# Kernel optimization log

Hardware: AMD Instinct MI355X
Metric: run time of the kernel (lower is better)

Reference implementation:

```python
import jax, jax.numpy as jnp
import numpy as np

N = 4096      # number of nodes/tokens (no batch dim in source)
D = 1024      # hidden_dim
H = 16        # n_heads
HD = D // H   # head_dim = 64
LN_EPS = 1e-5


def setup_inputs() -> dict:
    key = jax.random.key(0)
    ks = jax.random.split(key, 18)
    s = 0.02
    h = jax.random.normal(ks[0], (N, D), jnp.float32)
    rel_pos = jax.random.normal(ks[1], (N, N, 3), jnp.float32)
    # Linear weights stored (in, out) so y = x @ W + b (equiv to torch x @ W.T)
    Wq = jax.random.normal(ks[2], (D, D), jnp.float32) * s
    bq = jnp.zeros((D,), jnp.float32)
    Wk = jax.random.normal(ks[3], (D, D), jnp.float32) * s
    bk = jnp.zeros((D,), jnp.float32)
    Wv = jax.random.normal(ks[4], (D, D), jnp.float32) * s
    bv = jnp.zeros((D,), jnp.float32)
    Wo = jax.random.normal(ks[5], (D, D), jnp.float32) * s
    bo = jnp.zeros((D,), jnp.float32)
    # coord_mlp: Linear(D, D//2) -> SiLU -> Linear(D//2, 1)
    W1 = jax.random.normal(ks[6], (D, D // 2), jnp.float32) * s
    b1 = jnp.zeros((D // 2,), jnp.float32)
    W2 = jax.random.normal(ks[7], (D // 2, 1), jnp.float32) * s
    b2 = jnp.zeros((1,), jnp.float32)
    ln_w = jnp.ones((D,), jnp.float32)
    ln_b = jnp.zeros((D,), jnp.float32)
    return {"h": h, "rel_pos": rel_pos, "Wq": Wq, "bq": bq, "Wk": Wk, "bk": bk,
            "Wv": Wv, "bv": bv, "Wo": Wo, "bo": bo, "W1": W1, "b1": b1,
            "W2": W2, "b2": b2, "ln_w": ln_w, "ln_b": ln_b}


def reference(h, rel_pos, Wq, bq, Wk, bk, Wv, bv, Wo, bo, W1, b1, W2, b2, ln_w, ln_b):
    q = (h @ Wq + bq).reshape(-1, H, HD)
    k = (h @ Wk + bk).reshape(-1, H, HD)
    v = (h @ Wv + bv).reshape(-1, H, HD)
    scores = jnp.einsum('nhd,mhd->nmh', q, k) / np.sqrt(HD)  # [N, N, H]
    # Faithful to source: softmax over dim=-1 == the HEADS axis (quirk of the module)
    attn = jax.nn.softmax(scores, axis=-1)
    out = jnp.einsum('nmh,mhd->nhd', attn, v).reshape(-1, H * HD)
    out = out @ Wo + bo
    x = h + out
    mu = jnp.mean(x, axis=-1, keepdims=True)
    var = jnp.mean(jnp.square(x - mu), axis=-1, keepdims=True)
    hn = (x - mu) / jnp.sqrt(var + LN_EPS) * ln_w + ln_b
    coord_weights = jax.nn.silu(hn @ W1 + b1) @ W2 + b2   # [N, 1]
    pos_update = coord_weights * jnp.mean(rel_pos, axis=1)  # [N, 3]
    return (hn, pos_update)
```

## Files before the change

### kernel.cpp

```cpp
#include <hip/hip_runtime.h>

typedef __bf16 bf16x8 __attribute__((ext_vector_type(8)));
typedef float  f4     __attribute__((ext_vector_type(4)));
typedef unsigned short u16;
typedef unsigned short u16x4 __attribute__((ext_vector_type(4)));
typedef unsigned short u16x8 __attribute__((ext_vector_type(8)));

#define DEV __device__ __forceinline__

DEV u16 f2bf(float x) {
  unsigned u = __float_as_uint(x);
  unsigned r = u + 0x7FFFu + ((u >> 16) & 1u);
  return (u16)(r >> 16);
}
DEV float bf2f(u16 h) { return __uint_as_float(((unsigned)h) << 16); }

typedef const __attribute__((address_space(1))) void gv_t;
typedef __attribute__((address_space(3))) void lv_t;
DEV void g2l16(const void* g, void* l) {
  __builtin_amdgcn_global_load_lds((gv_t*)g, (lv_t*)l, 16, 0, 0);
}

__global__ void split_kernel(const float* __restrict__ src,
                             u16* __restrict__ hi, u16* __restrict__ lo) {
  size_t i = (size_t)blockIdx.x * 256 + threadIdx.x;
  float4 v = ((const float4*)src)[i];
  u16x4 h, l;
  u16 a;
  a = f2bf(v.x); h[0] = a; l[0] = f2bf(v.x - bf2f(a));
  a = f2bf(v.y); h[1] = a; l[1] = f2bf(v.y - bf2f(a));
  a = f2bf(v.z); h[2] = a; l[2] = f2bf(v.z - bf2f(a));
  a = f2bf(v.w); h[3] = a; l[3] = f2bf(v.w - bf2f(a));
  ((u16x4*)hi)[i] = h; ((u16x4*)lo)[i] = l;
}

__global__ void wsplit_t_kernel(const float* __restrict__ W,
                                u16* __restrict__ th, u16* __restrict__ tl, int J) {
  int j0 = blockIdx.x * 64, k0 = blockIdx.y * 64;
  __shared__ float tile[64][68];
  int t = threadIdx.x;
  int r16 = t >> 4, q = t & 15;
#pragma unroll
  for (int p = 0; p < 4; ++p) {
    int kk = r16 + p * 16;
    float4 v = *(const float4*)(W + (size_t)(k0 + kk) * J + j0 + q * 4);
    tile[kk][q * 4 + 0] = v.x; tile[kk][q * 4 + 1] = v.y;
    tile[kk][q * 4 + 2] = v.z; tile[kk][q * 4 + 3] = v.w;
  }
  __syncthreads();
  int rr = t >> 2, cq = t & 3;
  u16x8 h0, h1, l0, l1;
#pragma unroll
  for (int i = 0; i < 8; ++i) {
    float v = tile[cq * 16 + i][rr];
    u16 hh = f2bf(v); h0[i] = hh; l0[i] = f2bf(v - bf2f(hh));
    float v2 = tile[cq * 16 + 8 + i][rr];
    u16 hb = f2bf(v2); h1[i] = hb; l1[i] = f2bf(v2 - bf2f(hb));
  }
  size_t ob = (size_t)(j0 + rr) * 1024 + k0 + cq * 16;
  *(u16x8*)(th + ob) = h0; *(u16x8*)(th + ob + 8) = h1;
  *(u16x8*)(tl + ob) = l0; *(u16x8*)(tl + ob + 8) = l1;
}

template <int EPI>
__global__ __launch_bounds__(256, 2) void gemm_split_kernel(
    const u16* __restrict__ Ahi, const u16* __restrict__ Alo,
    const u16* __restrict__ Bthi, const u16* __restrict__ Btlo,
    float* __restrict__ Cf, u16* __restrict__ Cbf,
    const float* __restrict__ bias0, const float* __restrict__ bias1,
    const float* __restrict__ bias2, const float* __restrict__ Hres) {
  __shared__ alignas(16) u16 a_lds[2][4096];
  __shared__ alignas(16) u16 b_lds[2][4096];
  int t = threadIdx.x, l = t & 63, w = t >> 6;
  int wr = w >> 1, wc = w & 1, lr = l & 15, g = l >> 4;
  int m0 = blockIdx.y * 128, n0 = blockIdx.x * 128;

  f4 acc[4][4];
#pragma unroll
  for (int i = 0; i < 4; ++i)
#pragma unroll
    for (int j = 0; j < 4; ++j) acc[i][j] = (f4){0.f, 0.f, 0.f, 0.f};

  auto stage = [&](int s, int buf) {
    int p = s >> 5, k0 = (s & 31) * 32;
    const u16* As = (p < 2) ? Ahi : Alo;
    const u16* Bs = (p == 1) ? Btlo : Bthi;
#pragma unroll
    for (int i = 0; i < 2; ++i) {
      int idx = t + i * 256, r = idx >> 2, c = idx & 3;
      g2l16(As + (size_t)(m0 + r) * 1024 + k0 + 8 * (c ^ (r & 3)), &a_lds[buf][idx * 8]);
    }
#pragma unroll
    for (int i = 0; i < 2; ++i) {
      int idx = t + i * 256, r = idx >> 2, c = idx & 3;
      g2l16(Bs + (size_t)(n0 + r) * 1024 + k0 + 8 * (c ^ (r & 3)), &b_lds[buf][idx * 8]);
    }
  };

  stage(0, 0);
  for (int s = 0; s < 96; ++s) {
    __syncthreads();
    if (s + 1 < 96) stage(s + 1, (s + 1) & 1);
    const u16* ab = a_lds[s & 1];
    const u16* bb = b_lds[s & 1];
    bf16x8 af[4], bf[4];
#pragma unroll
    for (int mt = 0; mt < 4; ++mt) {
      int row = wr * 64 + mt * 16 + lr;
      af[mt] = *(const bf16x8*)(ab + row * 32 + 8 * (g ^ (row & 3)));
    }
#pragma unroll
    for (int nt = 0; nt < 4; ++nt) {
      int row = wc * 64 + nt * 16 + lr;
      bf[nt] = *(const bf16x8*)(bb + row * 32 + 8 * (g ^ (row & 3)));
    }
#pragma unroll
    for (int mt = 0; mt < 4; ++mt)
#pragma unroll
      for (int nt = 0; nt < 4; ++nt)
        acc[mt][nt] = __builtin_amdgcn_mfma_f32_16x16x32_bf16(af[mt], bf[nt], acc[mt][nt], 0, 0, 0);
  }

#pragma unroll
  for (int mt = 0; mt < 4; ++mt)
#pragma unroll
    for (int nt = 0; nt < 4; ++nt) {
      int col = n0 + wc * 64 + nt * 16 + lr;
#pragma unroll
      for (int r = 0; r < 4; ++r) {
        int row = m0 + wr * 64 + mt * 16 + 4 * g + r;
        float v = acc[mt][nt][r];
        if (EPI == 0) {
          float b = (col < 1024) ? bias0[col] : (col < 2048 ? bias1[col - 1024] : bias2[col - 2048]);
          v += b;
          if (col < 1024) v *= 0.125f;
          Cbf[(size_t)row * 3072 + col] = f2bf(v);
        } else if (EPI == 1) {
          v += bias0[col] + Hres[(size_t)row * 1024 + col];
          Cf[(size_t)row * 1024 + col] = v;
        } else {
          v += bias0[col];
          Cf[(size_t)row * 512 + col] = v;
        }
      }
    }
}

__global__ void kv_retile_kernel(const u16* __restrict__ qkvs,
                                 u16* __restrict__ kt, u16* __restrict__ vt2) {
  int mblk = blockIdx.x, t = threadIdx.x;
  __shared__ alignas(16) u16 lds[16][1032];
#pragma unroll
  for (int p = 0; p < 8; ++p) {
    int idx = t + p * 256, r = idx >> 7, c8 = idx & 127;
    *(u16x8*)(&lds[r][c8 * 8]) =
        *(const u16x8*)(qkvs + (size_t)(mblk * 16 + r) * 3072 + 1024 + c8 * 8);
  }
  __syncthreads();
#pragma unroll
  for (int p = 0; p < 8; ++p) {
    int ch = t + p * 256, cc = ch >> 4, m = ch & 15;
    u16x8 v = *(const u16x8*)(&lds[m][cc * 8]);
    *(u16x8*)(kt + (size_t)mblk * 16384 + cc * 128 + m * 8) = v;
  }
  __syncthreads();
#pragma unroll
  for (int p = 0; p < 8; ++p) {
    int idx = t + p * 256, r = idx >> 7, c8 = idx & 127;
    *(u16x8*)(&lds[r][c8 * 8]) =
        *(const u16x8*)(qkvs + (size_t)(mblk * 16 + r) * 3072 + 2048 + c8 * 8);
  }
  __syncthreads();
#pragma unroll
  for (int p = 0; p < 8; ++p) {
    int ch = t + p * 256, row = ch >> 1, half = ch & 1;
    u16x8 v;
#pragma unroll
    for (int i = 0; i < 8; ++i) v[i] = lds[half * 8 + i][row];
    *(u16x8*)(vt2 + (size_t)mblk * 16384 + row * 16 + half * 8) = v;
  }
}

__global__ __launch_bounds__(512, 2) void attn_kernel(
    const u16* __restrict__ qkvs, const u16* __restrict__ kt,
    const u16* __restrict__ vt2, float* __restrict__ out_part) {
  int t = threadIdx.x, l = t & 63, w = t >> 6;
  int nsub = w >> 2, grp = w & 3, lr = l & 15, g = l >> 4;
  int b = blockIdx.x, n0 = (b >> 1) * 32, mhalf = b & 1;
  int nrow = n0 + nsub * 16 + lr;

  __shared__ float zbuf[2][4][16][16];

  bf16x8 qf[4][2];
#pragma unroll
  for (int hh = 0; hh < 4; ++hh)
#pragma unroll
    for (int ks = 0; ks < 2; ++ks)
      qf[hh][ks] = *(const bf16x8*)(qkvs + (size_t)nrow * 3072 + (grp * 4 + hh) * 64 + ks * 32 + 8 * g);

  f4 oacc[4][4];
#pragma unroll
  for (int i = 0; i < 4; ++i)
#pragma unroll
    for (int j = 0; j < 4; ++j) oacc[i][j] = (f4){0.f, 0.f, 0.f, 0.f};

  float* opb = out_part + (size_t)mhalf * 1024 * 4096;

  for (int step = 0; step < 128; ++step) {
    int mblk = mhalf * 128 + step;
    const u16* ktb = kt + (size_t)mblk * 16384;
    const u16* vtb = vt2 + (size_t)mblk * 16384;

    u16x4 va[4][4];
#pragma unroll
    for (int hh = 0; hh < 4; ++hh)
#pragma unroll
      for (int dc = 0; dc < 4; ++dc) {
        int vrow = (grp * 4 + hh) * 64 + dc * 16 + lr;
        va[hh][dc] = *(const u16x4*)(vtb + vrow * 16 + 4 * g);
      }

    f4 sacc[4];
#pragma unroll
    for (int hh = 0; hh < 4; ++hh) sacc[hh] = (f4){0.f, 0.f, 0.f, 0.f};
#pragma unroll
    for (int ks = 0; ks < 2; ++ks) {
      bf16x8 kf[4];
#pragma unroll
      for (int hh = 0; hh < 4; ++hh) {
        int cc = (grp * 4 + hh) * 8 + ks * 4 + g;
        kf[hh] = *(const bf16x8*)(ktb + (cc * 16 + lr) * 8);
      }
#pragma unroll
      for (int hh = 0; hh < 4; ++hh)
        sacc[hh] = __builtin_amdgcn_mfma_f32_16x16x32_bf16(kf[hh], qf[hh][ks], sacc[hh], 0, 0, 0);
    }

    float ep[4][4], zp[4] = {0.f, 0.f, 0.f, 0.f};
#pragma unroll
    for (int hh = 0; hh < 4; ++hh)
#pragma unroll
      for (int r = 0; r < 4; ++r) {
        float e = __expf(sacc[hh][r]);
        ep[hh][r] = e; zp[r] += e;
      }
#pragma unroll
    for (int r = 0; r < 4; ++r) zbuf[nsub][grp][4 * g + r][lr] = zp[r];

    asm volatile("s_waitcnt lgkmcnt(0)" ::: "memory");
    __builtin_amdgcn_sched_barrier(0);
    __builtin_amdgcn_s_barrier();

    float invz[4];
#pragma unroll
    for (int r = 0; r < 4; ++r) {
      float z = zbuf[nsub][0][4 * g + r][lr] + zbuf[nsub][1][4 * g + r][lr] +
                zbuf[nsub][2][4 * g + r][lr] + zbuf[nsub][3][4 * g + r][lr];
      invz[r] = 1.0f / z;
    }

#pragma unroll
    for (int hh = 0; hh < 4; ++hh) {
      u16x8 pbu = (u16x8){0, 0, 0, 0, 0, 0, 0, 0};
      pbu[0] = f2bf(ep[hh][0] * invz[0]);
      pbu[1] = f2bf(ep[hh][1] * invz[1]);
      pbu[2] = f2bf(ep[hh][2] * invz[2]);
      pbu[3] = f2bf(ep[hh][3] * invz[3]);
      bf16x8 pb = __builtin_bit_cast(bf16x8, pbu);
#pragma unroll
      for (int dc = 0; dc < 4; ++dc) {
        u16x8 au = (u16x8){0, 0, 0, 0, 0, 0, 0, 0};
        au[0] = va[hh][dc][0]; au[1] = va[hh][dc][1];
        au[2] = va[hh][dc][2]; au[3] = va[hh][dc][3];
        bf16x8 af = __builtin_bit_cast(bf16x8, au);
        oacc[hh][dc] = __builtin_amdgcn_mfma_f32_16x16x32_bf16(af, pb, oacc[hh][dc], 0, 0, 0);
      }
    }
    asm volatile("s_waitcnt lgkmcnt(0)" ::: "memory");
    __builtin_amdgcn_sched_barrier(0);
    __builtin_amdgcn_s_barrier();
  }

#pragma unroll
  for (int hh = 0; hh < 4; ++hh)
#pragma unroll
    for (int dc = 0; dc < 4; ++dc)
#pragma unroll
      for (int r = 0; r < 4; ++r) {
        int c = (grp * 4 + hh) * 64 + dc * 16 + 4 * g + r;
        opb[(size_t)c * 4096 + nrow] = oacc[hh][dc][r];
      }
}

__global__ void combine_kernel(const float* __restrict__ part,
                               u16* __restrict__ aoh, u16* __restrict__ aol) {
  int n0 = blockIdx.x * 64, c0 = blockIdx.y * 64;
  __shared__ float tl[64][68];
  int t = threadIdx.x;
  int r16 = t >> 4, q = t & 15;
#pragma unroll
  for (int p = 0; p < 4; ++p) {
    int cc = r16 + p * 16;
    size_t off = (size_t)(c0 + cc) * 4096 + n0 + q * 4;
    float4 v0 = *(const float4*)(part + off);
    float4 v1 = *(const float4*)(part + 4194304u + off);
    tl[cc][q * 4 + 0] = v0.x + v1.x;
    tl[cc][q * 4 + 1] = v0.y + v1.y;
    tl[cc][q * 4 + 2] = v0.z + v1.z;
    tl[cc][q * 4 + 3] = v0.w + v1.w;
  }
  __syncthreads();
  int rr = t >> 2, cq = t & 3;
  u16x8 h0, h1, l0, l1;
#pragma unroll
  for (int i = 0; i < 8; ++i) {
    float v = tl[cq * 16 + i][rr];
    u16 hh = f2bf(v); h0[i] = hh; l0[i] = f2bf(v - bf2f(hh));
    float v2 = tl[cq * 16 + 8 + i][rr];
    u16 hb = f2bf(v2); h1[i] = hb; l1[i] = f2bf(v2 - bf2f(hb));
  }
  size_t ob = (size_t)(n0 + rr) * 1024 + c0 + cq * 16;
  *(u16x8*)(aoh + ob) = h0; *(u16x8*)(aoh + ob + 8) = h1;
  *(u16x8*)(aol + ob) = l0; *(u16x8*)(aol + ob + 8) = l1;
}

__global__ __launch_bounds__(256) void ln_kernel(
    const float* __restrict__ x, const float* __restrict__ lnw,
    const float* __restrict__ lnb, float* __restrict__ hn_out,
    u16* __restrict__ hnh, u16* __restrict__ hnl) {
  int row = blockIdx.x, t = threadIdx.x;
  const float* xr = x + (size_t)row * 1024;
  float4 v = *(const float4*)(xr + t * 4);
  float s = v.x + v.y + v.z + v.w;
  float sq = v.x * v.x + v.y * v.y + v.z * v.z + v.w * v.w;
#pragma unroll
  for (int o = 32; o > 0; o >>= 1) { s += __shfl_down(s, o); sq += __shfl_down(sq, o); }
  __shared__ float red[8];
  __shared__ float mv[2];
  if ((t & 63) == 0) { red[t >> 6] = s; red[4 + (t >> 6)] = sq; }
  __syncthreads();
  if (t == 0) {
    float S = red[0] + red[1] + red[2] + red[3];
    float Q = red[4] + red[5] + red[6] + red[7];
    float mu = S * (1.0f / 1024.0f);
    float var = Q * (1.0f / 1024.0f) - mu * mu;
    mv[0] = mu; mv[1] = rsqrtf(var + 1e-5f);
  }
  __syncthreads();
  float mu = mv[0], rstd = mv[1];
  float4 wv = *(const float4*)(lnw + t * 4);
  float4 bv = *(const float4*)(lnb + t * 4);
  float4 o;
  o.x = (v.x - mu) * rstd * wv.x + bv.x;
  o.y = (v.y - mu) * rstd * wv.y + bv.y;
  o.z = (v.z - mu) * rstd * wv.z + bv.z;
  o.w = (v.w - mu) * rstd * wv.w + bv.w;
  *(float4*)(hn_out + (size_t)row * 1024 + t * 4) = o;
  u16x4 hh, ll; u16 a;
  a = f2bf(o.x); hh[0] = a; ll[0] = f2bf(o.x - bf2f(a));
  a = f2bf(o.y); hh[1] = a; ll[1] = f2bf(o.y - bf2f(a));
  a = f2bf(o.z); hh[2] = a; ll[2] = f2bf(o.z - bf2f(a));
  a = f2bf(o.w); hh[3] = a; ll[3] = f2bf(o.w - bf2f(a));
  *(u16x4*)(hnh + (size_t)row * 1024 + t * 4) = hh;
  *(u16x4*)(hnl + (size_t)row * 1024 + t * 4) = ll;
}

__global__ __launch_bounds__(128) void cw_kernel(
    const float* __restrict__ g, const float* __restrict__ W2,
    const float* __restrict__ b2, float* __restrict__ cw) {
  int row = blockIdx.x, t = threadIdx.x;
  float4 v = *(const float4*)(g + (size_t)row * 512 + t * 4);
  float4 wv = *(const float4*)(W2 + t * 4);
  float s = (v.x / (1.0f + __expf(-v.x))) * wv.x + (v.y / (1.0f + __expf(-v.y))) * wv.y +
            (v.z / (1.0f + __expf(-v.z))) * wv.z + (v.w / (1.0f + __expf(-v.w))) * wv.w;
#pragma unroll
  for (int o = 32; o > 0; o >>= 1) s += __shfl_down(s, o);
  __shared__ float red[2];
  if ((t & 63) == 0) red[t >> 6] = s;
  __syncthreads();
  if (t == 0) cw[row] = red[0] + red[1] + b2[0];
}

__global__ __launch_bounds__(256) void rowmean_kernel(
    const float* __restrict__ rel, const float* __restrict__ cw,
    float* __restrict__ pu) {
  int n = blockIdx.x, t = threadIdx.x;
  const float* base = rel + (size_t)n * 12288;
  float a0 = 0.f, a1 = 0.f, a2 = 0.f;
#pragma unroll
  for (int it = 0; it < 12; ++it) {
    int e4 = it * 256 + t;
    float4 v = *(const float4*)(base + (size_t)e4 * 4);
    int rm = e4 % 3;
    if (rm == 0)      { a0 += v.x; a1 += v.y; a2 += v.z; a0 += v.w; }
    else if (rm == 1) { a1 += v.x; a2 += v.y; a0 += v.z; a1 += v.w; }
    else              { a2 += v.x; a0 += v.y; a1 += v.z; a2 += v.w; }
  }
#pragma unroll
  for (int o = 32; o > 0; o >>= 1) {
    a0 += __shfl_down(a0, o); a1 += __shfl_down(a1, o); a2 += __shfl_down(a2, o);
  }
  __shared__ float red[4][3];
  if ((t & 63) == 0) { red[t >> 6][0] = a0; red[t >> 6][1] = a1; red[t >> 6][2] = a2; }
  __syncthreads();
  if (t == 0) {
    float s0 = red[0][0] + red[1][0] + red[2][0] + red[3][0];
    float s1 = red[0][1] + red[1][1] + red[2][1] + red[3][1];
    float s2 = red[0][2] + red[1][2] + red[2][2] + red[3][2];
    float c = cw[n] * (1.0f / 4096.0f);
    pu[n * 3 + 0] = c * s0; pu[n * 3 + 1] = c * s1; pu[n * 3 + 2] = c * s2;
  }
}

extern "C" void kernel_launch(void* const* d_in, const int* in_sizes, int n_in,
                              void* d_out, int out_size, void* d_ws, size_t ws_size,
                              hipStream_t stream) {
  const float* h   = (const float*)d_in[0];
  const float* rel = (const float*)d_in[1];
  const float* Wq  = (const float*)d_in[2];
  const float* bq  = (const float*)d_in[3];
  const float* Wk  = (const float*)d_in[4];
  const float* bk  = (const float*)d_in[5];
  const float* Wv  = (const float*)d_in[6];
  const float* bv  = (const float*)d_in[7];
  const float* Wo  = (const float*)d_in[8];
  const float* bo  = (const float*)d_in[9];
  const float* W1  = (const float*)d_in[10];
  const float* b1  = (const float*)d_in[11];
  const float* W2  = (const float*)d_in[12];
  const float* b2  = (const float*)d_in[13];
  const float* lnw = (const float*)d_in[14];
  const float* lnb = (const float*)d_in[15];
  float* out_hn = (float*)d_out;
  float* out_pu = (float*)d_out + 4194304;

  char* ws = (char*)d_ws;
  u16*   wqkv_th = (u16*)(ws);
  u16*   wqkv_tl = (u16*)(ws + 6291456);
  u16*   wo_th   = (u16*)(ws + 12582912);
  u16*   wo_tl   = (u16*)(ws + 14680064);
  u16*   w1_th   = (u16*)(ws + 16777216);
  u16*   w1_tl   = (u16*)(ws + 17825792);
  u16*   h_hi    = (u16*)(ws + 18874368);
  u16*   h_lo    = (u16*)(ws + 27262976);
  u16*   qkvs    = (u16*)(ws + 35651584);
  u16*   ao_hi   = (u16*)(ws + 35651584);
  u16*   ao_lo   = (u16*)(ws + 44040192);
  u16*   kt      = (u16*)(ws + 60817408);
  u16*   vt2     = (u16*)(ws + 69206016);
  float* opart   = (float*)(ws + 77594624);
  float* xbuf    = (float*)(ws + 77594624);
  float* gbuf    = (float*)(ws + 94371840);
  float* cw      = (float*)(ws + 111149056);

  split_kernel<<<4096, 256, 0, stream>>>(h, h_hi, h_lo);
  wsplit_t_kernel<<<dim3(16, 16), 256, 0, stream>>>(Wq, wqkv_th, wqkv_tl, 1024);
  wsplit_t_kernel<<<dim3(16, 16), 256, 0, stream>>>(Wk, wqkv_th + 1048576, wqkv_tl + 1048576, 1024);
  wsplit_t_kernel<<<dim3(16, 16), 256, 0, stream>>>(Wv, wqkv_th + 2097152, wqkv_tl + 2097152, 1024);
  wsplit_t_kernel<<<dim3(16, 16), 256, 0, stream>>>(Wo, wo_th, wo_tl, 1024);
  wsplit_t_kernel<<<dim3(8, 16), 256, 0, stream>>>(W1, w1_th, w1_tl, 512);

  gemm_split_kernel<0><<<dim3(24, 32), 256, 0, stream>>>(
      h_hi, h_lo, wqkv_th, wqkv_tl, nullptr, qkvs, bq, bk, bv, nullptr);

  kv_retile_kernel<<<256, 256, 0, stream>>>(qkvs, kt, vt2);

  attn_kernel<<<256, 512, 0, stream>>>(qkvs, kt, vt2, opart);

  combine_kernel<<<dim3(64, 16), 256, 0, stream>>>(opart, ao_hi, ao_lo);

  gemm_split_kernel<1><<<dim3(8, 32), 256, 0, stream>>>(
      ao_hi, ao_lo, wo_th, wo_tl, xbuf, nullptr, bo, nullptr, nullptr, h);

  ln_kernel<<<4096, 256, 0, stream>>>(xbuf, lnw, lnb, out_hn, h_hi, h_lo);

  gemm_split_kernel<2><<<dim3(4, 32), 256, 0, stream>>>(
      h_hi, h_lo, w1_th, w1_tl, gbuf, nullptr, b1, nullptr, nullptr, nullptr);

  cw_kernel<<<4096, 128, 0, stream>>>(gbuf, W2, b2, cw);

  rowmean_kernel<<<4096, 256, 0, stream>>>(rel, cw, out_pu);
}
```

Measured before the change: 862.4 us.

## Restructure attention: 8-way key split, 2 heads per wave, bf16 partials

The attention kernel now splits the key dimension 8 ways across blocks (1024 blocks instead of 256), and each wave owns 2 heads over 32 query rows rather than 4 heads over 16 rows. The per-(n,m) head-sum normalizer is shared through a swizzled, double-buffered bf16 LDS buffer, which allows one barrier per 4 key blocks instead of two barriers per key block. Partial outputs are stored as bf16, and the combine kernel sums 8 partials. This aims for more parallelism and fewer barriers. In exchange it adds combine traffic and precision loss from the bf16 normalizer and the bf16 partials.

```diff
diff --git a/kernel.cpp b/kernel.cpp
--- a/kernel.cpp
+++ b/kernel.cpp
@@ -183,131 +183,156 @@
 
 __global__ __launch_bounds__(512, 2) void attn_kernel(
     const u16* __restrict__ qkvs, const u16* __restrict__ kt,
-    const u16* __restrict__ vt2, float* __restrict__ out_part) {
+    const u16* __restrict__ vt2, u16* __restrict__ opart) {
   int t = threadIdx.x, l = t & 63, w = t >> 6;
-  int nsub = w >> 2, grp = w & 3, lr = l & 15, g = l >> 4;
-  int b = blockIdx.x, n0 = (b >> 1) * 32, mhalf = b & 1;
-  int nrow = n0 + nsub * 16 + lr;
-
-  __shared__ float zbuf[2][4][16][16];
-
-  bf16x8 qf[4][2];
-#pragma unroll
-  for (int hh = 0; hh < 4; ++hh)
+  int lr = l & 15, g = l >> 4;
+  int b = blockIdx.x, me = b & 7, ng = b >> 3;
+  int n0 = ng * 32;
+  int head0 = w * 2;
+
+  __shared__ u16 zbuf[2][64 * 32 * 8];
+
+  bf16x8 qf[2][2][2];
+#pragma unroll
+  for (int h = 0; h < 2; ++h)
 #pragma unroll
     for (int ks = 0; ks < 2; ++ks)
-      qf[hh][ks] = *(const bf16x8*)(qkvs + (size_t)nrow * 3072 + (grp * 4 + hh) * 64 + ks * 32 + 8 * g);
-
-  f4 oacc[4][4];
-#pragma unroll
-  for (int i = 0; i < 4; ++i)
-#pragma unroll
-    for (int j = 0; j < 4; ++j) oacc[i][j] = (f4){0.f, 0.f, 0.f, 0.f};
-
-  float* opb = out_part + (size_t)mhalf * 1024 * 4096;
-
-  for (int step = 0; step < 128; ++step) {
-    int mblk = mhalf * 128 + step;
-    const u16* ktb = kt + (size_t)mblk * 16384;
-    const u16* vtb = vt2 + (size_t)mblk * 16384;
-
-    u16x4 va[4][4];
-#pragma unroll
-    for (int hh = 0; hh < 4; ++hh)
-#pragma unroll
-      for (int dc = 0; dc < 4; ++dc) {
-        int vrow = (grp * 4 + hh) * 64 + dc * 16 + lr;
-        va[hh][dc] = *(const u16x4*)(vtb + vrow * 16 + 4 * g);
-      }
-
-    f4 sacc[4];
-#pragma unroll
-    for (int hh = 0; hh < 4; ++hh) sacc[hh] = (f4){0.f, 0.f, 0.f, 0.f};
-#pragma unroll
-    for (int ks = 0; ks < 2; ++ks) {
-      bf16x8 kf[4];
-#pragma unroll
-      for (int hh = 0; hh < 4; ++hh) {
-        int cc = (grp * 4 + hh) * 8 + ks * 4 + g;
-        kf[hh] = *(const bf16x8*)(ktb + (cc * 16 + lr) * 8);
-      }
-#pragma unroll
-      for (int hh = 0; hh < 4; ++hh)
-        sacc[hh] = __builtin_amdgcn_mfma_f32_16x16x32_bf16(kf[hh], qf[hh][ks], sacc[hh], 0, 0, 0);
-    }
-
-    float ep[4][4], zp[4] = {0.f, 0.f, 0.f, 0.f};
-#pragma unroll
-    for (int hh = 0; hh < 4; ++hh)
-#pragma unroll
-      for (int r = 0; r < 4; ++r) {
-        float e = __expf(sacc[hh][r]);
-        ep[hh][r] = e; zp[r] += e;
-      }
-#pragma unroll
-    for (int r = 0; r < 4; ++r) zbuf[nsub][grp][4 * g + r][lr] = zp[r];
+#pragma unroll
+      for (int nt = 0; nt < 2; ++nt)
+        qf[h][ks][nt] = *(const bf16x8*)(
+            qkvs + (size_t)(n0 + nt * 16 + lr) * 3072 + (head0 + h) * 64 + ks * 32 + 8 * g);
+
+  f4 oacc[2][4][2];
+#pragma unroll
+  for (int h = 0; h < 2; ++h)
+#pragma unroll
+    for (int dc = 0; dc < 4; ++dc)
+#pragma unroll
+      for (int nt = 0; nt < 2; ++nt) oacc[h][dc][nt] = (f4){0.f, 0.f, 0.f, 0.f};
+
+  for (int ds = 0; ds < 8; ++ds) {
+    int mb0 = me * 32 + ds * 4;
+    int parity = ds & 1;
+    u16* zb = &zbuf[parity][0];
+
+    f4 ep[4][2][2];
+
+#pragma unroll
+    for (int j = 0; j < 4; ++j) {
+      const u16* ktb = kt + (size_t)(mb0 + j) * 16384;
+      f4 s[2][2];
+#pragma unroll
+      for (int h = 0; h < 2; ++h)
+#pragma unroll
+        for (int nt = 0; nt < 2; ++nt) s[h][nt] = (f4){0.f, 0.f, 0.f, 0.f};
+#pragma unroll
+      for (int h = 0; h < 2; ++h)
+#pragma unroll
+        for (int ks = 0; ks < 2; ++ks) {
+          int cc = (head0 + h) * 8 + ks * 4 + g;
+          bf16x8 kf = *(const bf16x8*)(ktb + (cc * 16 + lr) * 8);
+#pragma unroll
+          for (int nt = 0; nt < 2; ++nt)
+            s[h][nt] = __builtin_amdgcn_mfma_f32_16x16x32_bf16(kf, qf[h][ks][nt], s[h][nt], 0, 0, 0);
+        }
+#pragma unroll
+      for (int nt = 0; nt < 2; ++nt)
+#pragma unroll
+        for (int r = 0; r < 4; ++r) {
+          float e0 = __expf(s[0][nt][r]);
+          float e1 = __expf(s[1][nt][r]);
+          ep[j][0][nt][r] = e0;
+          ep[j][1][nt][r] = e1;
+          float zp = e0 + e1;
+          int m = j * 16 + 4 * g + r, n = nt * 16 + lr;
+          unsigned byte = (((unsigned)(m * 32 + n) * 16u) ^ (((unsigned)(m >> 2) & 3u) << 4)) +
+                          (unsigned)w * 2u;
+          *(u16*)((char*)zb + byte) = __builtin_bit_cast(u16, (__bf16)zp);
+        }
+    }
 
     asm volatile("s_waitcnt lgkmcnt(0)" ::: "memory");
     __builtin_amdgcn_sched_barrier(0);
     __builtin_amdgcn_s_barrier();
 
-    float invz[4];
-#pragma unroll
-    for (int r = 0; r < 4; ++r) {
-      float z = zbuf[nsub][0][4 * g + r][lr] + zbuf[nsub][1][4 * g + r][lr] +
-                zbuf[nsub][2][4 * g + r][lr] + zbuf[nsub][3][4 * g + r][lr];
-      invz[r] = 1.0f / z;
-    }
-
-#pragma unroll
-    for (int hh = 0; hh < 4; ++hh) {
-      u16x8 pbu = (u16x8){0, 0, 0, 0, 0, 0, 0, 0};
-      pbu[0] = f2bf(ep[hh][0] * invz[0]);
-      pbu[1] = f2bf(ep[hh][1] * invz[1]);
-      pbu[2] = f2bf(ep[hh][2] * invz[2]);
-      pbu[3] = f2bf(ep[hh][3] * invz[3]);
-      bf16x8 pb = __builtin_bit_cast(bf16x8, pbu);
-#pragma unroll
-      for (int dc = 0; dc < 4; ++dc) {
-        u16x8 au = (u16x8){0, 0, 0, 0, 0, 0, 0, 0};
-        au[0] = va[hh][dc][0]; au[1] = va[hh][dc][1];
-        au[2] = va[hh][dc][2]; au[3] = va[hh][dc][3];
-        bf16x8 af = __builtin_bit_cast(bf16x8, au);
-        oacc[hh][dc] = __builtin_amdgcn_mfma_f32_16x16x32_bf16(af, pb, oacc[hh][dc], 0, 0, 0);
-      }
-    }
-    asm volatile("s_waitcnt lgkmcnt(0)" ::: "memory");
-    __builtin_amdgcn_sched_barrier(0);
-    __builtin_amdgcn_s_barrier();
-  }
-
-#pragma unroll
-  for (int hh = 0; hh < 4; ++hh)
+#pragma unroll
+    for (int p = 0; p < 2; ++p) {
+      bf16x8 pb[2][2];
+#pragma unroll
+      for (int nt = 0; nt < 2; ++nt)
+#pragma unroll
+        for (int r = 0; r < 4; ++r) {
+          int n = nt * 16 + lr;
+          int mA = (2 * p) * 16 + 4 * g + r;
+          int mB = (2 * p + 1) * 16 + 4 * g + r;
+          unsigned byA = ((unsigned)(mA * 32 + n) * 16u) ^ (((unsigned)(mA >> 2) & 3u) << 4);
+          unsigned byB = ((unsigned)(mB * 32 + n) * 16u) ^ (((unsigned)(mB >> 2) & 3u) << 4);
+          u16x8 zA = *(const u16x8*)((const char*)zb + byA);
+          u16x8 zB = *(const u16x8*)((const char*)zb + byB);
+          float sA = 0.f, sB = 0.f;
+#pragma unroll
+          for (int k = 0; k < 8; ++k) { sA += bf2f(zA[k]); sB += bf2f(zB[k]); }
+          float rzA = __builtin_amdgcn_rcpf(sA);
+          float rzB = __builtin_amdgcn_rcpf(sB);
+          pb[0][nt][r]     = (__bf16)(ep[2 * p][0][nt][r] * rzA);
+          pb[0][nt][r + 4] = (__bf16)(ep[2 * p + 1][0][nt][r] * rzB);
+          pb[1][nt][r]     = (__bf16)(ep[2 * p][1][nt][r] * rzA);
+          pb[1][nt][r + 4] = (__bf16)(ep[2 * p + 1][1][nt][r] * rzB);
+        }
+      const u16* vtA = vt2 + (size_t)(mb0 + 2 * p) * 16384;
+      const u16* vtB = vt2 + (size_t)(mb0 + 2 * p + 1) * 16384;
+#pragma unroll
+      for (int h = 0; h < 2; ++h)
+#pragma unroll
+        for (int dc = 0; dc < 4; ++dc) {
+          int vrow = (head0 + h) * 64 + dc * 16 + lr;
+          u16x4 aA = *(const u16x4*)(vtA + vrow * 16 + 4 * g);
+          u16x4 aB = *(const u16x4*)(vtB + vrow * 16 + 4 * g);
+          u16x8 au;
+          au[0] = aA[0]; au[1] = aA[1]; au[2] = aA[2]; au[3] = aA[3];
+          au[4] = aB[0]; au[5] = aB[1]; au[6] = aB[2]; au[7] = aB[3];
+          bf16x8 af = __builtin_bit_cast(bf16x8, au);
+#pragma unroll
+          for (int nt = 0; nt < 2; ++nt)
+            oacc[h][dc][nt] =
+                __builtin_amdgcn_mfma_f32_16x16x32_bf16(af, pb[h][nt], oacc[h][dc][nt], 0, 0, 0);
+        }
+    }
+  }
+
+  u16* opb = opart + (size_t)me * 4194304;
+#pragma unroll
+  for (int h = 0; h < 2; ++h)
 #pragma unroll
     for (int dc = 0; dc < 4; ++dc)
 #pragma unroll
-      for (int r = 0; r < 4; ++r) {
-        int c = (grp * 4 + hh) * 64 + dc * 16 + 4 * g + r;
-        opb[(size_t)c * 4096 + nrow] = oacc[hh][dc][r];
-      }
-}
-
-__global__ void combine_kernel(const float* __restrict__ part,
+      for (int nt = 0; nt < 2; ++nt)
+#pragma unroll
+        for (int r = 0; r < 4; ++r) {
+          int c = (head0 + h) * 64 + dc * 16 + 4 * g + r;
+          int n = n0 + nt * 16 + lr;
+          opb[(size_t)c * 4096 + n] = f2bf(oacc[h][dc][nt][r]);
+        }
+}
+
+__global__ void combine_kernel(const u16* __restrict__ part,
                                u16* __restrict__ aoh, u16* __restrict__ aol) {
   int n0 = blockIdx.x * 64, c0 = blockIdx.y * 64;
   __shared__ float tl[64][68];
   int t = threadIdx.x;
-  int r16 = t >> 4, q = t & 15;
-#pragma unroll
-  for (int p = 0; p < 4; ++p) {
-    int cc = r16 + p * 16;
-    size_t off = (size_t)(c0 + cc) * 4096 + n0 + q * 4;
-    float4 v0 = *(const float4*)(part + off);
-    float4 v1 = *(const float4*)(part + 4194304u + off);
-    tl[cc][q * 4 + 0] = v0.x + v1.x;
-    tl[cc][q * 4 + 1] = v0.y + v1.y;
-    tl[cc][q * 4 + 2] = v0.z + v1.z;
-    tl[cc][q * 4 + 3] = v0.w + v1.w;
+  int q = t & 7, row = t >> 3;
+#pragma unroll
+  for (int it = 0; it < 2; ++it) {
+    int cc = row + it * 32;
+    float s[8] = {0.f, 0.f, 0.f, 0.f, 0.f, 0.f, 0.f, 0.f};
+#pragma unroll
+    for (int p = 0; p < 8; ++p) {
+      u16x8 v = *(const u16x8*)(part + (size_t)p * 4194304 + (size_t)(c0 + cc) * 4096 + n0 + q * 8);
+#pragma unroll
+      for (int j = 0; j < 8; ++j) s[j] += bf2f(v[j]);
+    }
+#pragma unroll
+    for (int j = 0; j < 8; ++j) tl[cc][q * 8 + j] = s[j];
   }
   __syncthreads();
   int rr = t >> 2, cq = t & 3;
@@ -448,7 +473,7 @@
   u16*   ao_lo   = (u16*)(ws + 44040192);
   u16*   kt      = (u16*)(ws + 60817408);
   u16*   vt2     = (u16*)(ws + 69206016);
-  float* opart   = (float*)(ws + 77594624);
+  u16*   opart   = (u16*)(ws + 77594624);
   float* xbuf    = (float*)(ws + 77594624);
   float* gbuf    = (float*)(ws + 94371840);
   float* cw      = (float*)(ws + 111149056);
@@ -465,7 +490,7 @@
 
   kv_retile_kernel<<<256, 256, 0, stream>>>(qkvs, kt, vt2);
 
-  attn_kernel<<<256, 512, 0, stream>>>(qkvs, kt, vt2, opart);
+  attn_kernel<<<1024, 512, 0, stream>>>(qkvs, kt, vt2, opart);
 
   combine_kernel<<<dim3(64, 16), 256, 0, stream>>>(opart, ao_hi, ao_lo);
 
```

New measurement: 886.6 us. +2.8%, slower.
